# Performance work log

Measured on AMD Instinct MI355X. Metric: run time of the kernel, lower is better.

The kernel has to match this reference:

```python
import jax, jax.numpy as jnp
import numpy as np

N, T, C = 2048, 1024, 24
MAX_PAIRS = 256
ALPHAS = (1.0 / 3.0, 1.0 / 3.0, 1.0 / 3.0)


def setup_inputs() -> dict:
    key = jax.random.key(0)
    k1, k2, k3 = jax.random.split(key, 3)
    logits = jax.random.normal(k1, (N, T, C), dtype=jnp.float32)
    log_class_probabilities = jax.nn.log_softmax(logits, axis=-1)
    y_true = jax.random.randint(k2, (N, T), 0, C, dtype=jnp.int32)
    # per-sample stopping time in [1, T); timestamps_left counts down to 0 at t_stop
    t_stop = jax.random.randint(k3, (N,), 1, T)
    t = jnp.arange(T)
    timestamps_left = jnp.maximum(t_stop[:, None] - t[None, :], 0).astype(jnp.float32)
    return {
        "log_class_probabilities": log_class_probabilities,
        "timestamps_left": timestamps_left,
        "y_true": y_true,
    }


def _loss(logp, timestamps_left, y_true):
    n, t_len, c = logp.shape
    dt = logp.dtype
    # --- classification loss: NLL per (n,t), sum over T, mean over N ---
    logp_true = jnp.take_along_axis(logp, y_true[..., None].astype(jnp.int32), axis=2)[..., 0]  # (N,T)
    classification_loss = (-logp_true).sum(axis=1).mean(axis=0)
    # --- earliness reward ---
    t = jnp.arange(t_len, dtype=dt)
    p_correct = jnp.exp(logp_true)  # probability_correct_class
    earliness_reward = (p_correct * (1.0 - t / t_len) * (1.0 - timestamps_left / t_len)).sum(axis=1).mean(axis=0)
    # --- proximity reward (vectorized per-class pairwise, capped at MAX_PAIRS pairs/class) ---
    t_final = jnp.argmax(timestamps_left <= 0, axis=1)  # get_t_stop_from_daily_timestamps, (N,)
    cls = y_true[:, 0]  # targets[:, 0]
    v = jnp.exp(logp[jnp.arange(n), t_final, cls])  # exp(logprob at t_final, true-class channel), (N,)
    onehot = jax.nn.one_hot(cls, c, dtype=jnp.int32)  # (N,C)
    rank = jnp.cumsum(onehot, axis=0)[jnp.arange(n), cls] - 1  # rank of sample within its class (index order)
    size = onehot.sum(axis=0)[cls]  # class size per sample, (N,)
    a = rank[:, None]
    b = rank[None, :]
    same_class = cls[:, None] == cls[None, :]
    # torch.combinations lexicographic pair index; keep first MAX_PAIRS pairs per class
    combo_idx = a * size[:, None] - a * (a + 1) // 2 + (b - a - 1)
    sel = same_class & (a < b) & (combo_idx < MAX_PAIRS)
    dtf = (t_final[:, None] - t_final[None, :]).astype(dt) / t_len
    proximity_reward = jnp.sum(jnp.where(sel, (v[:, None] * v[None, :]) * dtf * dtf, jnp.zeros((), dt)))
    return ALPHAS[0] * classification_loss - ALPHAS[1] * earliness_reward - ALPHAS[2] * proximity_reward


def reference(log_class_probabilities, timestamps_left, y_true):
    return _loss(log_class_probabilities, timestamps_left, y_true)
```

## Files before the change

### kernel.cpp

```cpp
#include <hip/hip_runtime.h>
#include <hip/hip_bf16.h>
#include <math.h>

#define NN 2048
#define TT 1024
#define CC 24
#define MAXP 256


__global__ __launch_bounds__(256) void k_main(const float* __restrict__ logp,
                                              const float* __restrict__ tlft,
                                              const int* __restrict__ yt,
                                              float* __restrict__ pcls,
                                              float* __restrict__ pearl) {
    const float invT = 1.0f / (float)TT;
    float s_cls = 0.0f, s_earl = 0.0f;
    const int total = NN * TT;
    const int stride = gridDim.x * blockDim.x;
    for (int idx = blockIdx.x * blockDim.x + threadIdx.x; idx < total; idx += stride) {
        int y = yt[idx];
        float lp = logp[(size_t)idx * CC + y];
        float tl = tlft[idx];
        int t = idx & (TT - 1);
        s_cls += -lp;
        s_earl += expf(lp) * (1.0f - (float)t * invT) * (1.0f - tl * invT);
    }
    for (int off = 32; off; off >>= 1) {
        s_cls  += __shfl_down(s_cls,  off);
        s_earl += __shfl_down(s_earl, off);
    }
    __shared__ float l1[4], l2[4];
    int wid = threadIdx.x >> 6, lane = threadIdx.x & 63;
    if (lane == 0) { l1[wid] = s_cls; l2[wid] = s_earl; }
    __syncthreads();
    if (threadIdx.x == 0) {
        float a = 0.f, b = 0.f;
        for (int w = 0; w < 4; ++w) { a += l1[w]; b += l2[w]; }
        pcls[blockIdx.x] = a;
        pearl[blockIdx.x] = b;
    }
}

__global__ __launch_bounds__(64) void k_tfinal(const float* __restrict__ logp,
                                               const float* __restrict__ tlft,
                                               const int* __restrict__ yt,
                                               int* __restrict__ tfin,
                                               int* __restrict__ clsA,
                                               float* __restrict__ vA) {
    int n = blockIdx.x;
    int lane = threadIdx.x;
    const float* row = tlft + (size_t)n * TT;
    int m = TT;
    for (int t = lane; t < TT; t += 64)
        if (row[t] <= 0.0f && t < m) m = t;
    for (int off = 32; off; off >>= 1) {
        int o = __shfl_down(m, off);
        if (o < m) m = o;
    }
    if (lane == 0) {
        if (m == TT) m = 0;
        int c = yt[(size_t)n * TT];
        float v = expf(logp[((size_t)n * TT + m) * CC + c]);
        tfin[n] = m;
        clsA[n] = c;
        vA[n]   = v;
    }
}

__global__ __launch_bounds__(256) void k_prox2(const int* __restrict__ clsA,
                                               const int* __restrict__ tfin,
                                               const float* __restrict__ vA,
                                               float* __restrict__ pprox) {
    __shared__ int   s_tf[NN];
    __shared__ float s_v[NN];
    __shared__ int   s_cnt[256];
    __shared__ int   s_off[257];
    const int c = blockIdx.x;
    const int tid = threadIdx.x;
    const int base = tid * 8;

    int flags[8];
    int cnt = 0;
#pragma unroll
    for (int k = 0; k < 8; ++k) {
        int match = (clsA[base + k] == c) ? 1 : 0;
        flags[k] = match;
        cnt += match;
    }
    s_cnt[tid] = cnt;
    __syncthreads();
    if (tid == 0) {
        int run = 0;
        for (int i = 0; i < 256; ++i) { s_off[i] = run; run += s_cnt[i]; }
        s_off[256] = run;
    }
    __syncthreads();
    int off = s_off[tid];
#pragma unroll
    for (int k = 0; k < 8; ++k) {
        if (flags[k]) {
            int n = base + k;
            s_tf[off] = tfin[n];
            s_v[off]  = vA[n];
            ++off;
        }
    }
    __syncthreads();

    const int S = s_off[256];
    const long long totalPairs = (long long)S * (S - 1) / 2;
    const int lim = (int)(totalPairs < MAXP ? totalPairs : MAXP);
    const float invT = 1.0f / (float)TT;
    float acc = 0.0f;
    for (int combo = tid; combo < lim; combo += 256) {
        int a = 0, b0 = 0;
        for (;;) {
            int cA = S - 1 - a;
            if (combo < b0 + cA) break;
            b0 += cA; ++a;
        }
        int b = a + 1 + (combo - b0);
        float dtf = (float)(s_tf[a] - s_tf[b]) * invT;
        acc += s_v[a] * s_v[b] * dtf * dtf;
    }
    for (int o = 32; o; o >>= 1) acc += __shfl_down(acc, o);
    __shared__ float lp[4];
    int wid = tid >> 6, lane = tid & 63;
    if (lane == 0) lp[wid] = acc;
    __syncthreads();
    if (tid == 0) {
        float s = 0.f;
        for (int w = 0; w < 4; ++w) s += lp[w];
        pprox[blockIdx.x] = s;
    }
}

__global__ __launch_bounds__(256) void k_final(const float* __restrict__ pcls,
                                               const float* __restrict__ pearl,
                                               const float* __restrict__ pprox,
                                               float* __restrict__ out) {
    double c = 0.0, e = 0.0;
    for (int i = threadIdx.x; i < 2048; i += 256) { c += (double)pcls[i]; e += (double)pearl[i]; }
    for (int off = 32; off; off >>= 1) {
        c += __shfl_down(c, off);
        e += __shfl_down(e, off);
    }
    __shared__ double lc[4], le[4];
    int wid = threadIdx.x >> 6, lane = threadIdx.x & 63;
    if (lane == 0) { lc[wid] = c; le[wid] = e; }
    __syncthreads();
    if (threadIdx.x == 0) {
        double cs = 0.0, es = 0.0;
        for (int w = 0; w < 4; ++w) { cs += lc[w]; es += le[w]; }
        double p = 0.0;
        for (int i = 0; i < CC; ++i) p += (double)pprox[i];
        double loss = (cs / (double)NN) * (1.0 / 3.0)
                    - (es / (double)NN) * (1.0 / 3.0)
                    - p * (1.0 / 3.0);
        out[0] = (float)loss;
    }
}

extern "C" void kernel_launch(void* const* d_in, const int* in_sizes, int n_in,
                              void* d_out, int out_size, void* d_ws, size_t ws_size,
                              hipStream_t stream) {
    const float* logp = (const float*)d_in[0];
    const float* tlft = (const float*)d_in[1];
    const int*   yt   = (const int*)d_in[2];
    float* out = (float*)d_out;

    char* ws = (char*)d_ws;
    float* pcls  = (float*)(ws + 0);
    float* pearl = (float*)(ws + 8192);
    int*   tfin  = (int*)  (ws + 16384);
    int*   clsA  = (int*)  (ws + 24576);
    float* vA    = (float*)(ws + 32768);
    float* pprox = (float*)(ws + 40960);

    k_main  <<<2048, 256, 0, stream>>>(logp, tlft, yt, pcls, pearl);
    k_tfinal<<<2048,  64, 0, stream>>>(logp, tlft, yt, tfin, clsA, vA);
    k_prox2 <<<  CC, 256, 0, stream>>>(clsA, tfin, vA, pprox);
    k_final <<<   1, 256, 0, stream>>>(pcls, pearl, pprox, out);
}
```

Measured before the change: 300.7 us.

## Fuse stop-time search into main pass and merge proximity with final reduction

The main per-row kernel now also computes each sample's stop index, class and stop probability, so the separate t_final kernel no longer re-reads timestamps_left. The per-class proximity kernel and the final reduction are merged into one 1024-thread block that compacts classes with ballot/popcount and gives each class to one wavefront. This removes two kernel launches and one extra pass over timestamps_left. The cost is that the tail stage now runs on a single block, with serialized per-class work.

```diff
diff --git a/kernel.cpp b/kernel.cpp
--- a/kernel.cpp
+++ b/kernel.cpp
@@ -8,152 +8,146 @@
 #define MAXP 256
 
 
-__global__ __launch_bounds__(256) void k_main(const float* __restrict__ logp,
-                                              const float* __restrict__ tlft,
-                                              const int* __restrict__ yt,
-                                              float* __restrict__ pcls,
-                                              float* __restrict__ pearl) {
+__global__ __launch_bounds__(256) void k_fused(const float* __restrict__ logp,
+                                               const float* __restrict__ tlft,
+                                               const int* __restrict__ yt,
+                                               float* __restrict__ pcls,
+                                               float* __restrict__ pearl,
+                                               int* __restrict__ tfin,
+                                               int* __restrict__ clsA,
+                                               float* __restrict__ vA) {
+    const int n = blockIdx.x;
+    const int tid = threadIdx.x;
     const float invT = 1.0f / (float)TT;
+    const size_t rowbase = (size_t)n * TT;
+
     float s_cls = 0.0f, s_earl = 0.0f;
-    const int total = NN * TT;
-    const int stride = gridDim.x * blockDim.x;
-    for (int idx = blockIdx.x * blockDim.x + threadIdx.x; idx < total; idx += stride) {
+    int m = TT;
+#pragma unroll
+    for (int k = 0; k < 4; ++k) {
+        int t = tid + k * 256;
+        size_t idx = rowbase + t;
         int y = yt[idx];
-        float lp = logp[(size_t)idx * CC + y];
         float tl = tlft[idx];
-        int t = idx & (TT - 1);
-        s_cls += -lp;
+        float lp = logp[idx * CC + y];
+        s_cls -= lp;
         s_earl += expf(lp) * (1.0f - (float)t * invT) * (1.0f - tl * invT);
+        if (tl <= 0.0f && t < m) m = t;
     }
     for (int off = 32; off; off >>= 1) {
         s_cls  += __shfl_down(s_cls,  off);
         s_earl += __shfl_down(s_earl, off);
+        int o = __shfl_down(m, off);
+        if (o < m) m = o;
     }
     __shared__ float l1[4], l2[4];
-    int wid = threadIdx.x >> 6, lane = threadIdx.x & 63;
-    if (lane == 0) { l1[wid] = s_cls; l2[wid] = s_earl; }
+    __shared__ int   lm[4];
+    int wid = tid >> 6, lane = tid & 63;
+    if (lane == 0) { l1[wid] = s_cls; l2[wid] = s_earl; lm[wid] = m; }
     __syncthreads();
-    if (threadIdx.x == 0) {
-        float a = 0.f, b = 0.f;
-        for (int w = 0; w < 4; ++w) { a += l1[w]; b += l2[w]; }
-        pcls[blockIdx.x] = a;
-        pearl[blockIdx.x] = b;
+    if (tid == 0) {
+        float a = 0.f, b = 0.f; int mm = TT;
+        for (int w = 0; w < 4; ++w) {
+            a += l1[w]; b += l2[w];
+            if (lm[w] < mm) mm = lm[w];
+        }
+        if (mm == TT) mm = 0;
+        int c = yt[rowbase];
+        pcls[n]  = a;
+        pearl[n] = b;
+        tfin[n]  = mm;
+        clsA[n]  = c;
+        vA[n]    = expf(logp[(rowbase + mm) * CC + c]);
     }
 }
 
-__global__ __launch_bounds__(64) void k_tfinal(const float* __restrict__ logp,
-                                               const float* __restrict__ tlft,
-                                               const int* __restrict__ yt,
-                                               int* __restrict__ tfin,
-                                               int* __restrict__ clsA,
-                                               float* __restrict__ vA) {
-    int n = blockIdx.x;
-    int lane = threadIdx.x;
-    const float* row = tlft + (size_t)n * TT;
-    int m = TT;
-    for (int t = lane; t < TT; t += 64)
-        if (row[t] <= 0.0f && t < m) m = t;
-    for (int off = 32; off; off >>= 1) {
-        int o = __shfl_down(m, off);
-        if (o < m) m = o;
-    }
-    if (lane == 0) {
-        if (m == TT) m = 0;
-        int c = yt[(size_t)n * TT];
-        float v = expf(logp[((size_t)n * TT + m) * CC + c]);
-        tfin[n] = m;
-        clsA[n] = c;
-        vA[n]   = v;
-    }
-}
-
-__global__ __launch_bounds__(256) void k_prox2(const int* __restrict__ clsA,
+__global__ __launch_bounds__(1024) void k_tail(const float* __restrict__ pcls,
+                                               const float* __restrict__ pearl,
+                                               const int* __restrict__ clsA,
                                                const int* __restrict__ tfin,
                                                const float* __restrict__ vA,
-                                               float* __restrict__ pprox) {
-    __shared__ int   s_tf[NN];
-    __shared__ float s_v[NN];
-    __shared__ int   s_cnt[256];
-    __shared__ int   s_off[257];
-    const int c = blockIdx.x;
-    const int tid = threadIdx.x;
-    const int base = tid * 8;
+                                               float* __restrict__ out) {
+    __shared__ int    s_cls[NN];
+    __shared__ int    s_mtf[NN];
+    __shared__ float  s_mv[NN];
+    __shared__ int    s_csize[CC];
+    __shared__ int    s_coff[CC];
+    __shared__ float  s_ppart[CC];
+    __shared__ double lc[16], le[16];
 
-    int flags[8];
-    int cnt = 0;
-#pragma unroll
-    for (int k = 0; k < 8; ++k) {
-        int match = (clsA[base + k] == c) ? 1 : 0;
-        flags[k] = match;
-        cnt += match;
-    }
-    s_cnt[tid] = cnt;
-    __syncthreads();
-    if (tid == 0) {
-        int run = 0;
-        for (int i = 0; i < 256; ++i) { s_off[i] = run; run += s_cnt[i]; }
-        s_off[256] = run;
-    }
-    __syncthreads();
-    int off = s_off[tid];
-#pragma unroll
-    for (int k = 0; k < 8; ++k) {
-        if (flags[k]) {
-            int n = base + k;
-            s_tf[off] = tfin[n];
-            s_v[off]  = vA[n];
-            ++off;
-        }
-    }
-    __syncthreads();
+    const int tid  = threadIdx.x;
+    const int wid  = tid >> 6;
+    const int lane = tid & 63;
 
-    const int S = s_off[256];
-    const long long totalPairs = (long long)S * (S - 1) / 2;
-    const int lim = (int)(totalPairs < MAXP ? totalPairs : MAXP);
-    const float invT = 1.0f / (float)TT;
-    float acc = 0.0f;
-    for (int combo = tid; combo < lim; combo += 256) {
-        int a = 0, b0 = 0;
-        for (;;) {
-            int cA = S - 1 - a;
-            if (combo < b0 + cA) break;
-            b0 += cA; ++a;
-        }
-        int b = a + 1 + (combo - b0);
-        float dtf = (float)(s_tf[a] - s_tf[b]) * invT;
-        acc += s_v[a] * s_v[b] * dtf * dtf;
-    }
-    for (int o = 32; o; o >>= 1) acc += __shfl_down(acc, o);
-    __shared__ float lp[4];
-    int wid = tid >> 6, lane = tid & 63;
-    if (lane == 0) lp[wid] = acc;
-    __syncthreads();
-    if (tid == 0) {
-        float s = 0.f;
-        for (int w = 0; w < 4; ++w) s += lp[w];
-        pprox[blockIdx.x] = s;
-    }
-}
-
-__global__ __launch_bounds__(256) void k_final(const float* __restrict__ pcls,
-                                               const float* __restrict__ pearl,
-                                               const float* __restrict__ pprox,
-                                               float* __restrict__ out) {
-    double c = 0.0, e = 0.0;
-    for (int i = threadIdx.x; i < 2048; i += 256) { c += (double)pcls[i]; e += (double)pearl[i]; }
+    double c = (double)pcls[tid] + (double)pcls[tid + 1024];
+    double e = (double)pearl[tid] + (double)pearl[tid + 1024];
     for (int off = 32; off; off >>= 1) {
         c += __shfl_down(c, off);
         e += __shfl_down(e, off);
     }
-    __shared__ double lc[4], le[4];
-    int wid = threadIdx.x >> 6, lane = threadIdx.x & 63;
     if (lane == 0) { lc[wid] = c; le[wid] = e; }
+
+    s_cls[tid] = clsA[tid];
+    s_cls[tid + 1024] = clsA[tid + 1024];
+    if (tid < CC) s_ppart[tid] = 0.0f;
     __syncthreads();
-    if (threadIdx.x == 0) {
+
+    for (int cc = wid; cc < CC; cc += 16) {
+        int cnt = 0;
+        for (int chunk = 0; chunk < NN / 64; ++chunk) {
+            bool f = (s_cls[chunk * 64 + lane] == cc);
+            unsigned long long mask = __ballot(f);
+            cnt += __popcll(mask);
+        }
+        if (lane == 0) s_csize[cc] = cnt;
+    }
+    __syncthreads();
+    if (tid == 0) {
+        int run = 0;
+        for (int i = 0; i < CC; ++i) { s_coff[i] = run; run += s_csize[i]; }
+    }
+    __syncthreads();
+
+    const float invT = 1.0f / (float)TT;
+    for (int cc = wid; cc < CC; cc += 16) {
+        int base = s_coff[cc];
+        const int S = s_csize[cc];
+        for (int chunk = 0; chunk < NN / 64; ++chunk) {
+            int nidx = chunk * 64 + lane;
+            bool f = (s_cls[nidx] == cc);
+            unsigned long long mask = __ballot(f);
+            if (f) {
+                int pos = base + __popcll(mask & ((1ULL << lane) - 1ULL));
+                s_mtf[pos] = tfin[nidx];
+                s_mv[pos]  = vA[nidx];
+            }
+            base += __popcll(mask);
+        }
+        long long totalPairs = (long long)S * (S - 1) / 2;
+        int lim = (int)(totalPairs < MAXP ? totalPairs : MAXP);
+        int cbase = s_coff[cc];
+        float acc = 0.0f;
+        for (int combo = lane; combo < lim; combo += 64) {
+            int a = 0, b0 = 0;
+            for (;;) {
+                int cA = S - 1 - a;
+                if (combo < b0 + cA) break;
+                b0 += cA; ++a;
+            }
+            int b = a + 1 + (combo - b0);
+            float dtf = (float)(s_mtf[cbase + a] - s_mtf[cbase + b]) * invT;
+            acc += s_mv[cbase + a] * s_mv[cbase + b] * dtf * dtf;
+        }
+        for (int off = 32; off; off >>= 1) acc += __shfl_down(acc, off);
+        if (lane == 0) s_ppart[cc] = acc;
+    }
+    __syncthreads();
+
+    if (tid == 0) {
         double cs = 0.0, es = 0.0;
-        for (int w = 0; w < 4; ++w) { cs += lc[w]; es += le[w]; }
+        for (int w = 0; w < 16; ++w) { cs += lc[w]; es += le[w]; }
         double p = 0.0;
-        for (int i = 0; i < CC; ++i) p += (double)pprox[i];
+        for (int i = 0; i < CC; ++i) p += (double)s_ppart[i];
         double loss = (cs / (double)NN) * (1.0 / 3.0)
                     - (es / (double)NN) * (1.0 / 3.0)
                     - p * (1.0 / 3.0);
@@ -175,10 +169,7 @@
     int*   tfin  = (int*)  (ws + 16384);
     int*   clsA  = (int*)  (ws + 24576);
     float* vA    = (float*)(ws + 32768);
-    float* pprox = (float*)(ws + 40960);
 
-    k_main  <<<2048, 256, 0, stream>>>(logp, tlft, yt, pcls, pearl);
-    k_tfinal<<<2048,  64, 0, stream>>>(logp, tlft, yt, tfin, clsA, vA);
-    k_prox2 <<<  CC, 256, 0, stream>>>(clsA, tfin, vA, pprox);
-    k_final <<<   1, 256, 0, stream>>>(pcls, pearl, pprox, out);
+    k_fused<<<NN, 256, 0, stream>>>(logp, tlft, yt, pcls, pearl, tfin, clsA, vA);
+    k_tail <<< 1, 1024, 0, stream>>>(pcls, pearl, clsA, tfin, vA, out);
 }
```

Measured after the change: 297.3 us. No clear change (-1.1%).
